# Performance work log

Measured on AMD Instinct MI355X. Metric: run time of the kernel, lower is better.

The kernel has to match this reference:

```python
import jax, jax.numpy as jnp
import numpy as np

DIM = 192          # token dim
INNER = 288        # round4(1.5*DIM)
NH_Q = 72          # headwise-proj heads (INNER // qkv_block_size)
DH_Q = 4           # per-head dim of q/k/v projections
NH_M = 4           # mLSTM heads (= qkv_block_size)
DH_M = 72          # INNER // NH_M
H, W = 32, 32
S = H * W
B = 8
KS = 3             # conv kernel size
EPS = 1e-6
LN_EPS = 1e-5


def setup_inputs() -> dict:
    key = jax.random.key(0)
    ks = jax.random.split(key, 12)
    sc = 0.02
    return {
        "x": jax.random.normal(ks[0], (B, S, DIM), jnp.float32),
        "proj_up_w": jax.random.normal(ks[1], (2 * INNER, DIM), jnp.float32) * sc,
        "q_w": jax.random.normal(ks[2], (NH_Q, DH_Q, DH_Q), jnp.float32) * sc,
        "k_w": jax.random.normal(ks[3], (NH_Q, DH_Q, DH_Q), jnp.float32) * sc,
        "v_w": jax.random.normal(ks[4], (NH_Q, DH_Q, DH_Q), jnp.float32) * sc,
        "conv_w": jax.random.normal(ks[5], (KS, KS, 1, INNER), jnp.float32) * sc,  # depthwise HWIO
        "ig_w": jax.random.normal(ks[6], (NH_M, 3 * INNER), jnp.float32) * sc,
        "ig_b": jax.random.normal(ks[7], (NH_M,), jnp.float32) * 0.1,
        "fg_w": jax.random.normal(ks[8], (NH_M, 3 * INNER), jnp.float32) * sc,
        "fg_b": jnp.linspace(3.0, 6.0, NH_M, dtype=jnp.float32),  # original fgate bias init
        "norm_w": jnp.ones((INNER,), jnp.float32),
        "skip": jnp.ones((INNER,), jnp.float32),
        "proj_down_w": jax.random.normal(ks[9], (DIM, INNER), jnp.float32) * sc,
    }


def _headwise(x, w):
    # x: (B,S,INNER), w: (NH_Q, DH_Q, DH_Q); block-diagonal linear per head
    xh = x.reshape(*x.shape[:-1], NH_Q, DH_Q)
    return jnp.einsum("bshd,hod->bsho", xh, w).reshape(x.shape)


def _mlstm_parallel(q, k, v, ig, fg):
    # q,k,v: (B,NH,S,DH); ig,fg: (B,NH,S) gate preactivations
    Ss, DH = q.shape[2], q.shape[3]
    logf = jax.nn.log_sigmoid(fg)                 # (B,NH,S)
    lfc = jnp.cumsum(logf, axis=-1)               # (B,NH,S)
    logF = lfc[..., :, None] - lfc[..., None, :]  # (B,NH,S,S): sum of logf over (j, i]
    mask = jnp.tril(jnp.ones((Ss, Ss), bool))
    logD = jnp.where(mask, logF + ig[..., None, :], -jnp.inf)
    maxD = jnp.max(logD, axis=-1, keepdims=True)  # (B,NH,S,1)
    Dm = jnp.exp(logD - maxD)
    qk = jnp.einsum("bnsd,bntd->bnst", q, k) / jnp.sqrt(jnp.float32(DH))
    Cm = qk * Dm
    normalizer = jnp.maximum(jnp.abs(Cm.sum(-1, keepdims=True)), jnp.exp(-maxD))
    return jnp.einsum("bnst,bntd->bnsd", Cm / (normalizer + EPS), v)


def reference(x, proj_up_w, q_w, k_w, v_w, conv_w, ig_w, ig_b, fg_w, fg_b,
              norm_w, skip, proj_down_w):
    Bb, Ss, _ = x.shape
    y = x @ proj_up_w.T                               # (B,S,2*INNER)
    x_m, z = y[..., :INNER], y[..., INNER:]
    # depthwise 2d conv over the (H,W) token grid
    xc = x_m.reshape(Bb, H, W, INNER)
    xc = jax.lax.conv_general_dilated(
        xc, conv_w, (1, 1), "SAME",
        dimension_numbers=("NHWC", "HWIO", "NHWC"), feature_group_count=INNER)
    xc = xc.reshape(Bb, Ss, INNER)
    xa = jax.nn.silu(xc)
    q = _headwise(xa, q_w)
    k = _headwise(xa, k_w)
    v = _headwise(x_m, v_w)
    gate_in = jnp.concatenate([q, k, v], axis=-1)      # (B,S,3*INNER)
    ig = (gate_in @ ig_w.T + ig_b).transpose(0, 2, 1)  # (B,NH_M,S)
    fg = (gate_in @ fg_w.T + fg_b).transpose(0, 2, 1)
    qh = q.reshape(Bb, Ss, NH_M, DH_M).transpose(0, 2, 1, 3)
    kh = k.reshape(Bb, Ss, NH_M, DH_M).transpose(0, 2, 1, 3)
    vh = v.reshape(Bb, Ss, NH_M, DH_M).transpose(0, 2, 1, 3)
    h = _mlstm_parallel(qh, kh, vh, ig, fg)            # (B,NH_M,S,DH_M)
    # per-head layernorm (group norm with NH_M groups), weight per channel
    mu = h.mean(-1, keepdims=True)
    var = h.var(-1, keepdims=True)
    hn = (h - mu) / jnp.sqrt(var + LN_EPS)
    hn = hn * norm_w.reshape(NH_M, 1, DH_M)[None]
    hn = hn.transpose(0, 2, 1, 3).reshape(Bb, Ss, INNER)
    h_skip = hn + skip * xa
    h_state = h_skip * jax.nn.silu(z)
    return h_state @ proj_down_w.T
```

## Files before the change

kernel.cpp:

```cpp
#include <hip/hip_runtime.h>
#include <math.h>

#define B_ 8
#define S_ 1024
#define INNER_ 288
#define NHM_ 4
#define DHM_ 72
#define H_ 32
#define W_ 32

typedef unsigned short ushort_t;
typedef unsigned int uint_t;
typedef __bf16 bf16x8 __attribute__((ext_vector_type(8)));
typedef float f32x4 __attribute__((ext_vector_type(4)));

__device__ __forceinline__ ushort_t f2bf(float f) {
  union { float f; unsigned u; } v; v.f = f;
  unsigned r = v.u + 0x7FFF + ((v.u >> 16) & 1);
  return (ushort_t)(r >> 16);
}
__device__ __forceinline__ float bf2f(ushort_t u) {
  union { unsigned u; float f; } v; v.u = ((unsigned)u) << 16;
  return v.f;
}
__device__ __forceinline__ void gl16(const void* g, void* l) {
  __builtin_amdgcn_global_load_lds(
      (const __attribute__((address_space(1))) void*)g,
      (__attribute__((address_space(3))) void*)l, 16, 0, 0);
}

__global__ __launch_bounds__(256) void prep_kernel(
    const float* __restrict__ x, const float* __restrict__ wupf,
    const float* __restrict__ wdnf,
    ushort_t* __restrict__ xbf, ushort_t* __restrict__ wup, ushort_t* __restrict__ wdn,
    ushort_t* __restrict__ hsb, ushort_t* __restrict__ qg, ushort_t* __restrict__ kg) {
  int s4 = blockIdx.x * 256 + threadIdx.x;
  const ushort4 z4 = {0, 0, 0, 0};
  if (s4 < 393216) {
    const int m = s4 / 48, k4 = (s4 % 48) * 4;
    const float4 v = *(const float4*)&x[(size_t)m * 192 + k4];
    ushort4 w = {f2bf(v.x), f2bf(v.y), f2bf(v.z), f2bf(v.w)};
    *(ushort4*)&xbf[(size_t)m * 192 + (k4 & ~63) + ((k4 & 63) ^ ((m & 7) << 3))] = w;
    return;
  }
  s4 -= 393216;
  if (s4 < 27648) {
    const int m = s4 / 48, k4 = (s4 % 48) * 4;
    const float4 v = *(const float4*)&wupf[(size_t)m * 192 + k4];
    ushort4 w = {f2bf(v.x), f2bf(v.y), f2bf(v.z), f2bf(v.w)};
    *(ushort4*)&wup[(size_t)m * 192 + (k4 & ~63) + ((k4 & 63) ^ ((m & 7) << 3))] = w;
    return;
  }
  s4 -= 27648;
  if (s4 < 15360) {
    const int m = s4 / 80, k4 = (s4 % 80) * 4;
    ushort4 w = z4;
    if (k4 < 288) {
      const float4 v = *(const float4*)&wdnf[(size_t)m * 288 + k4];
      w = (ushort4){f2bf(v.x), f2bf(v.y), f2bf(v.z), f2bf(v.w)};
    }
    *(ushort4*)&wdn[(size_t)m * 320 + (k4 & ~63) + ((k4 & 63) ^ ((m & 7) << 3))] = w;
    return;
  }
  s4 -= 15360;
  if (s4 < 131072) {
    const int p = s4 >> 4, j = s4 & 15;
    *(ushort4*)&hsb[(size_t)p * 320 + 256 + j * 4] = z4;
    return;
  }
  s4 -= 131072;
  if (s4 < 524288) {
    const int r = s4 >> 4, j = s4 & 15;
    *(ushort4*)&qg[(size_t)r * 128 + 64 + j * 4] = z4;
    return;
  }
  s4 -= 524288;
  {
    const int r = s4 >> 4, j = s4 & 15;
    *(ushort4*)&kg[(size_t)r * 128 + 64 + j * 4] = z4;
  }
}

template<int KT>
__global__ __launch_bounds__(256) void gemm_bf16(
    const ushort_t* __restrict__ A, const ushort_t* __restrict__ Bw,
    float* __restrict__ C, int N) {
  __shared__ __align__(16) ushort_t As[2][128 * 64];
  __shared__ __align__(16) ushort_t Bs[2][64 * 64];
  const int tid = threadIdx.x, lane = tid & 63, wv = tid >> 6;
  const int wm = wv >> 1, wn = wv & 1;
  const int cl = lane & 15, rowb = lane >> 4;
  const int m0 = blockIdx.y * 128, n0 = blockIdx.x * 64;
  const char* Ab = (const char*)A;
  const char* Bb = (const char*)Bw;

  auto stage = [&](int buf, int kt) {
    for (int u = wv; u < 24; u += 4) {
      if (u < 16) {
        const int o = u * 1024 + lane * 16;
        const int r = o >> 7, c = o & 127;
        gl16(Ab + ((size_t)(m0 + r) * KT + kt) * 128 + c, (char*)As[buf] + u * 1024);
      } else {
        const int o = (u - 16) * 1024 + lane * 16;
        const int r = o >> 7, c = o & 127;
        gl16(Bb + ((size_t)(n0 + r) * KT + kt) * 128 + c, (char*)Bs[buf] + (u - 16) * 1024);
      }
    }
  };

  f32x4 acc[4][2];
#pragma unroll
  for (int mi = 0; mi < 4; ++mi)
#pragma unroll
    for (int nj = 0; nj < 2; ++nj) acc[mi][nj] = (f32x4){0.f, 0.f, 0.f, 0.f};

  stage(0, 0);
  __syncthreads();
  for (int kt = 0; kt < KT; ++kt) {
    const int cur = kt & 1;
    if (kt + 1 < KT) stage(cur ^ 1, kt + 1);
#pragma unroll
    for (int ks = 0; ks < 2; ++ks) {
      bf16x8 af[4], bfr[2];
#pragma unroll
      for (int mi = 0; mi < 4; ++mi) {
        const int row = wm * 64 + mi * 16 + cl;
        af[mi] = *(const bf16x8*)((const char*)As[cur] + row * 128 +
                                  ((2 * (ks * 32 + rowb * 8)) ^ ((row & 7) << 4)));
      }
#pragma unroll
      for (int nj = 0; nj < 2; ++nj) {
        const int row = wn * 32 + nj * 16 + cl;
        bfr[nj] = *(const bf16x8*)((const char*)Bs[cur] + row * 128 +
                                   ((2 * (ks * 32 + rowb * 8)) ^ ((row & 7) << 4)));
      }
#pragma unroll
      for (int mi = 0; mi < 4; ++mi)
#pragma unroll
        for (int nj = 0; nj < 2; ++nj)
          acc[mi][nj] = __builtin_amdgcn_mfma_f32_16x16x32_bf16(af[mi], bfr[nj], acc[mi][nj], 0, 0, 0);
    }
    __syncthreads();
  }
#pragma unroll
  for (int mi = 0; mi < 4; ++mi)
#pragma unroll
    for (int i = 0; i < 4; ++i) {
      const size_t m = m0 + wm * 64 + mi * 16 + rowb * 4 + i;
#pragma unroll
      for (int nj = 0; nj < 2; ++nj)
        C[m * N + n0 + wn * 32 + nj * 16 + cl] = acc[mi][nj][i];
    }
}

__global__ __launch_bounds__(256) void conv_head_kernel(
    const float* __restrict__ y, const float* __restrict__ cw,
    const float* __restrict__ qw, const float* __restrict__ kw, const float* __restrict__ vw,
    float* __restrict__ xa,
    ushort_t* __restrict__ qg, ushort_t* __restrict__ kg, ushort_t* __restrict__ vg) {
  const int idx = blockIdx.x * 256 + threadIdx.x;
  const int hq = idx % 72;
  const int p = idx / 72;
  const int c = hq * 4;
  const int xx = p & 31, yy = (p >> 5) & 31, b = p >> 10, s = p & 1023;
  float4 acc = {0.f, 0.f, 0.f, 0.f};
  float4 xmv;
#pragma unroll
  for (int ky = 0; ky < 3; ++ky) {
    const int iy = yy + ky - 1;
    if (iy < 0 || iy >= H_) continue;
#pragma unroll
    for (int kx = 0; kx < 3; ++kx) {
      const int ix = xx + kx - 1;
      if (ix < 0 || ix >= W_) continue;
      const float4 v = *(const float4*)&y[((size_t)((b << 10) + (iy << 5) + ix)) * 576 + c];
      if (ky == 1 && kx == 1) xmv = v;
      const float4 w = *(const float4*)&cw[(ky * 3 + kx) * INNER_ + c];
      acc.x += v.x * w.x; acc.y += v.y * w.y; acc.z += v.z * w.z; acc.w += v.w * w.w;
    }
  }
  float4 xa4;
  xa4.x = acc.x / (1.f + __expf(-acc.x));
  xa4.y = acc.y / (1.f + __expf(-acc.y));
  xa4.z = acc.z / (1.f + __expf(-acc.z));
  xa4.w = acc.w / (1.f + __expf(-acc.w));
  *(float4*)&xa[(size_t)p * INNER_ + c] = xa4;
  float q[4], k2[4], v[4];
#pragma unroll
  for (int o = 0; o < 4; ++o) {
    const float4 wq = *(const float4*)&qw[hq * 16 + o * 4];
    const float4 wk = *(const float4*)&kw[hq * 16 + o * 4];
    const float4 wv4 = *(const float4*)&vw[hq * 16 + o * 4];
    q[o]  = wq.x * xa4.x + wq.y * xa4.y + wq.z * xa4.z + wq.w * xa4.w;
    k2[o] = wk.x * xa4.x + wk.y * xa4.y + wk.z * xa4.z + wk.w * xa4.w;
    v[o]  = wv4.x * xmv.x + wv4.y * xmv.y + wv4.z * xmv.z + wv4.w * xmv.w;
  }
  const int n = hq / 18, g = hq % 18;
  const int r = (b * 4 + n) * 1024 + s;
  const int swz = (s & 7) << 3;
  ushort4 uq = {f2bf(q[0]), f2bf(q[1]), f2bf(q[2]), f2bf(q[3])};
  ushort4 uk = {f2bf(k2[0]), f2bf(k2[1]), f2bf(k2[2]), f2bf(k2[3])};
  ushort4 uv = {f2bf(v[0]), f2bf(v[1]), f2bf(v[2]), f2bf(v[3])};
  *(ushort4*)&qg[(size_t)r * 128 + ((g * 4) ^ swz)] = uq;
  *(ushort4*)&kg[(size_t)r * 128 + ((g * 4) ^ swz)] = uk;
  *(ushort4*)&vg[(size_t)r * 72 + g * 4] = uv;
}

__global__ __launch_bounds__(256) void vtrans_kernel(
    const ushort_t* __restrict__ vg, ushort_t* __restrict__ vtg) {
  __shared__ ushort_t T[64][82];
  const int bn = blockIdx.x >> 4, tt = blockIdx.x & 15;
  const int s0 = tt << 6, tid = threadIdx.x;
  const uint_t* v32 = (const uint_t*)vg;
  for (int i = tid; i < 64 * 36; i += 256) {
    const int rr = i / 36, c2 = i % 36;
    *(uint_t*)&T[rr][c2 * 2] = v32[((size_t)(bn * 1024 + s0 + rr)) * 36 + c2];
  }
  __syncthreads();
  char* outb = (char*)(vtg + ((size_t)(bn * 16 + tt)) * 5120);
  for (int i = tid; i < 80 * 32; i += 256) {
    const int d = i >> 5, m = i & 31;
    uint_t val;
    if (d < 72) val = (uint_t)T[2 * m][d] | ((uint_t)T[2 * m + 1][d] << 16);
    else val = (d == 72) ? 0x3F803F80u : 0u;
    *(uint_t*)(outb + d * 128 + ((m * 4) ^ ((d & 7) << 4))) = val;
  }
}

__global__ __launch_bounds__(256) void gates_kernel(
    const ushort_t* __restrict__ qg, const ushort_t* __restrict__ kg, const ushort_t* __restrict__ vg,
    const float* __restrict__ igw, const float* __restrict__ igb,
    const float* __restrict__ fgw, const float* __restrict__ fgb,
    float* __restrict__ ig, float* __restrict__ fg) {
  const int gw = (blockIdx.x * 256 + threadIdx.x) >> 6;
  const int lane = threadIdx.x & 63;
  const int b = gw >> 10, s = gw & 1023;
  float iacc[4] = {}, facc[4] = {};
  for (int j = lane; j < 864; j += 64) {
    const int part = j / INNER_;
    const int c = j - part * INNER_;
    const int n = c / DHM_, d = c % DHM_;
    const size_t row = (size_t)(b * 4 + n) * 1024 + s;
    ushort_t u;
    if (part == 2)      u = vg[row * 72 + d];
    else {
      const size_t si = row * 128 + (d ^ ((row & 7) << 3));
      u = (part == 0) ? qg[si] : kg[si];
    }
    const float gv = bf2f(u);
#pragma unroll
    for (int nn = 0; nn < 4; ++nn) {
      iacc[nn] += gv * igw[nn * 864 + j];
      facc[nn] += gv * fgw[nn * 864 + j];
    }
  }
#pragma unroll
  for (int off = 32; off >= 1; off >>= 1) {
#pragma unroll
    for (int nn = 0; nn < 4; ++nn) {
      iacc[nn] += __shfl_xor(iacc[nn], off);
      facc[nn] += __shfl_xor(facc[nn], off);
    }
  }
  if (lane == 0) {
#pragma unroll
    for (int nn = 0; nn < 4; ++nn) {
      ig[((size_t)b * NHM_ + nn) * S_ + s] = iacc[nn] + igb[nn];
      fg[((size_t)b * NHM_ + nn) * S_ + s] = facc[nn] + fgb[nn];
    }
  }
}

__global__ __launch_bounds__(256) void scan_kernel(
    const float* __restrict__ fg, const float* __restrict__ ig,
    float* __restrict__ lfc, float* __restrict__ g, float* __restrict__ Mb) {
  __shared__ float sd[256];
  const int bn = blockIdx.x;
  const int tid = threadIdx.x;
  const float* fgp = &fg[(size_t)bn * S_];
  const float* igp = &ig[(size_t)bn * S_];
  float lf[4];
#pragma unroll
  for (int i = 0; i < 4; ++i) {
    const float f = fgp[tid * 4 + i];
    lf[i] = (f >= 0.f) ? -log1pf(expf(-f)) : (f - log1pf(expf(f)));
  }
  float p[4];
  p[0] = lf[0]; p[1] = p[0] + lf[1]; p[2] = p[1] + lf[2]; p[3] = p[2] + lf[3];
  sd[tid] = p[3];
  __syncthreads();
  for (int off = 1; off < 256; off <<= 1) {
    const float v = (tid >= off) ? sd[tid - off] : 0.f;
    __syncthreads();
    sd[tid] += v;
    __syncthreads();
  }
  const float excl = sd[tid] - p[3];
  float l[4];
#pragma unroll
  for (int i = 0; i < 4; ++i) {
    l[i] = excl + p[i];
    lfc[(size_t)bn * S_ + tid * 4 + i] = l[i];
  }
  float gv[4], pm[4];
#pragma unroll
  for (int i = 0; i < 4; ++i) gv[i] = igp[tid * 4 + i] - l[i];
  pm[0] = gv[0];
#pragma unroll
  for (int i = 1; i < 4; ++i) pm[i] = fmaxf(pm[i - 1], gv[i]);
  __syncthreads();
  sd[tid] = pm[3];
  __syncthreads();
  for (int off = 1; off < 256; off <<= 1) {
    const float v = (tid >= off) ? sd[tid - off] : -INFINITY;
    __syncthreads();
    sd[tid] = fmaxf(sd[tid], v);
    __syncthreads();
  }
  const float exclm = (tid > 0) ? sd[tid - 1] : -INFINITY;
#pragma unroll
  for (int i = 0; i < 4; ++i) {
    g[(size_t)bn * S_ + tid * 4 + i] = gv[i];
    Mb[(size_t)bn * S_ + tid * 4 + i] = fmaxf(exclm, pm[i]);
  }
}

__global__ __launch_bounds__(256) void mlstm_mfma(
    const ushort_t* __restrict__ qg, const ushort_t* __restrict__ kg,
    const ushort_t* __restrict__ vtg,
    const float* __restrict__ gb, const float* __restrict__ Mb, const float* __restrict__ lfc,
    const float* __restrict__ xa, const float* __restrict__ y,
    const float* __restrict__ normw, const float* __restrict__ skipw,
    ushort_t* __restrict__ hsb) {
  __shared__ __align__(16) ushort_t Ks[2][64 * 128];
  __shared__ __align__(16) ushort_t Vt[2][80 * 64];
  __shared__ __align__(16) ushort_t Ps[64 * 72];
  __shared__ float gs[1024];
  __shared__ float Ms_s[64], en_s[64];
  const int bi = blockIdx.x;
  const int bn = bi & 31;
  const int j = (bi >> 5) & 7;
  const int st = (bi >> 8) ? (15 - j) : j;
  const int s0 = st << 6;
  const int tid = threadIdx.x, lane = tid & 63, wv = tid >> 6;
  const int cl = lane & 15, rowb = lane >> 4;
  const char* kb = (const char*)(kg + (size_t)bn * 1024 * 128);
  const char* vtb = (const char*)(vtg + (size_t)bn * 16 * 5120);

  auto stage = [&](int buf, int tt) {
    const char* ks = kb + (size_t)tt * (64 * 256);
    const char* vs = vtb + (size_t)tt * 10240;
    for (int u = wv; u < 26; u += 4) {
      if (u < 16) gl16(ks + u * 1024 + lane * 16, (char*)Ks[buf] + u * 1024);
      else        gl16(vs + (u - 16) * 1024 + lane * 16, (char*)Vt[buf] + (u - 16) * 1024);
    }
  };

  stage(0, 0);
  *(float4*)&gs[tid * 4] = *(const float4*)&gb[(size_t)bn * S_ + tid * 4];
  if (tid < 64) {
    const float m = Mb[(size_t)bn * S_ + s0 + tid];
    Ms_s[tid] = m;
    en_s[tid] = __expf(-(lfc[(size_t)bn * S_ + s0 + tid] + m));
  }
  const int qrow = bn * 1024 + s0 + 16 * wv + cl;
  const ushort_t* qp = qg + (size_t)qrow * 128;
  const int qx = (qrow & 7) << 3;
  bf16x8 qf[3];
#pragma unroll
  for (int kk = 0; kk < 3; ++kk) qf[kk] = *(const bf16x8*)&qp[(kk * 32 + rowb * 8) ^ qx];

  f32x4 accv[5];
#pragma unroll
  for (int n0 = 0; n0 < 5; ++n0) accv[n0] = (f32x4){0.f, 0.f, 0.f, 0.f};
  const float rsc = 0.11785113019775793f;
  const int srl0 = 16 * wv + 4 * rowb;
  __syncthreads();

  for (int tt = 0; tt < st; ++tt) {
    const int cur = tt & 1;
    stage(cur ^ 1, tt + 1);
    const int t0 = tt << 6;
    f32x4 qk[4];
#pragma unroll
    for (int n0 = 0; n0 < 4; ++n0) qk[n0] = (f32x4){0.f, 0.f, 0.f, 0.f};
#pragma unroll
    for (int kk = 0; kk < 3; ++kk) {
#pragma unroll
      for (int n0 = 0; n0 < 4; ++n0) {
        const int rl = n0 * 16 + cl;
        const bf16x8 b = *(const bf16x8*)((const char*)Ks[cur] + rl * 256 +
                                          ((2 * (kk * 32 + rowb * 8)) ^ ((rl & 7) << 4)));
        qk[n0] = __builtin_amdgcn_mfma_f32_16x16x32_bf16(qf[kk], b, qk[n0], 0, 0, 0);
      }
    }
#pragma unroll
    for (int n0 = 0; n0 < 4; ++n0) {
      const float gtv = gs[t0 + n0 * 16 + cl];
#pragma unroll
      for (int i = 0; i < 4; ++i) {
        const float w = qk[n0][i] * rsc * __expf(gtv - Ms_s[srl0 + i]);
        Ps[(srl0 + i) * 72 + n0 * 16 + cl] = f2bf(w);
      }
    }
#pragma unroll
    for (int k0 = 0; k0 < 64; k0 += 32) {
      const bf16x8 a = *(const bf16x8*)&Ps[(16 * wv + cl) * 72 + k0 + rowb * 8];
#pragma unroll
      for (int n0 = 0; n0 < 5; ++n0) {
        const int d = n0 * 16 + cl;
        const bf16x8 b = *(const bf16x8*)((const char*)Vt[cur] + d * 128 +
                                          ((2 * (k0 + rowb * 8)) ^ ((d & 7) << 4)));
        accv[n0] = __builtin_amdgcn_mfma_f32_16x16x32_bf16(a, b, accv[n0], 0, 0, 0);
      }
    }
    __syncthreads();
  }
  {
    const int cur = st & 1;
    f32x4 qk[4];
#pragma unroll
    for (int n0 = 0; n0 < 4; ++n0) qk[n0] = (f32x4){0.f, 0.f, 0.f, 0.f};
#pragma unroll
    for (int kk = 0; kk < 3; ++kk) {
#pragma unroll
      for (int n0 = 0; n0 < 4; ++n0) {
        const int rl = n0 * 16 + cl;
        const bf16x8 b = *(const bf16x8*)((const char*)Ks[cur] + rl * 256 +
                                          ((2 * (kk * 32 + rowb * 8)) ^ ((rl & 7) << 4)));
        qk[n0] = __builtin_amdgcn_mfma_f32_16x16x32_bf16(qf[kk], b, qk[n0], 0, 0, 0);
      }
    }
#pragma unroll
    for (int n0 = 0; n0 < 4; ++n0) {
      const int tc = n0 * 16 + cl;
      const float gtv = gs[s0 + tc];
#pragma unroll
      for (int i = 0; i < 4; ++i) {
        const int srl = srl0 + i;
        const float w = (tc <= srl) ? qk[n0][i] * rsc * __expf(gtv - Ms_s[srl]) : 0.f;
        Ps[srl * 72 + n0 * 16 + cl] = f2bf(w);
      }
    }
#pragma unroll
    for (int k0 = 0; k0 < 64; k0 += 32) {
      const bf16x8 a = *(const bf16x8*)&Ps[(16 * wv + cl) * 72 + k0 + rowb * 8];
#pragma unroll
      for (int n0 = 0; n0 < 5; ++n0) {
        const int d = n0 * 16 + cl;
        const bf16x8 b = *(const bf16x8*)((const char*)Vt[cur] + d * 128 +
                                          ((2 * (k0 + rowb * 8)) ^ ((d & 7) << 4)));
        accv[n0] = __builtin_amdgcn_mfma_f32_16x16x32_bf16(a, b, accv[n0], 0, 0, 0);
      }
    }
  }
  float inv[4];
#pragma unroll
  for (int i = 0; i < 4; ++i) {
    const float rs = __shfl(accv[4][i], (lane & 48) + 8, 64);
    inv[i] = 1.f / (fmaxf(fabsf(rs), en_s[srl0 + i]) + 1e-6f);
  }
  const int b = bn >> 2, n = bn & 3;
  float nw[5], sw[5];
#pragma unroll
  for (int n0 = 0; n0 < 5; ++n0) {
    const int d = n0 * 16 + cl;
    nw[n0] = (d < 72) ? normw[n * 72 + d] : 0.f;
    sw[n0] = (d < 72) ? skipw[n * 72 + d] : 0.f;
  }
#pragma unroll
  for (int i = 0; i < 4; ++i) {
    const int srl = srl0 + i;
    const int p = (b << 10) + s0 + srl;
    float hv[5];
#pragma unroll
    for (int n0 = 0; n0 < 5; ++n0) hv[n0] = accv[n0][i] * inv[i];
    float hsum = hv[0] + hv[1] + hv[2] + hv[3] + ((cl < 8) ? hv[4] : 0.f);
#pragma unroll
    for (int m = 1; m < 16; m <<= 1) hsum += __shfl_xor(hsum, m);
    const float mean = hsum * (1.f / 72.f);
    float dsq = 0.f;
#pragma unroll
    for (int n0 = 0; n0 < 5; ++n0) {
      const int d = n0 * 16 + cl;
      const float dd = hv[n0] - mean;
      if (d < 72) dsq += dd * dd;
    }
#pragma unroll
    for (int m = 1; m < 16; m <<= 1) dsq += __shfl_xor(dsq, m);
    const float rstd = rsqrtf(dsq * (1.f / 72.f) + 1e-5f);
    const int pswz = (p & 7) << 3;
#pragma unroll
    for (int n0 = 0; n0 < 5; ++n0) {
      const int d = n0 * 16 + cl;
      if (d < 72) {
        const int c = n * 72 + d;
        const float hn = (hv[n0] - mean) * rstd * nw[n0];
        const float xav = xa[(size_t)p * INNER_ + c];
        const float z = y[(size_t)p * 576 + 288 + c];
        const float sz = z / (1.f + __expf(-z));
        hsb[(size_t)p * 320 + (c & ~63) + ((c & 63) ^ pswz)] = f2bf((hn + sw[n0] * xav) * sz);
      }
    }
  }
}

extern "C" void kernel_launch(void* const* d_in, const int* in_sizes, int n_in,
                              void* d_out, int out_size, void* d_ws, size_t ws_size,
                              hipStream_t stream) {
  const float* x           = (const float*)d_in[0];
  const float* proj_up_w   = (const float*)d_in[1];
  const float* q_w         = (const float*)d_in[2];
  const float* k_w         = (const float*)d_in[3];
  const float* v_w         = (const float*)d_in[4];
  const float* conv_w      = (const float*)d_in[5];
  const float* ig_w        = (const float*)d_in[6];
  const float* ig_b        = (const float*)d_in[7];
  const float* fg_w        = (const float*)d_in[8];
  const float* fg_b        = (const float*)d_in[9];
  const float* norm_w      = (const float*)d_in[10];
  const float* skipw       = (const float*)d_in[11];
  const float* proj_down_w = (const float*)d_in[12];
  float* out = (float*)d_out;

  float* ws = (float*)d_ws;
  float* y      = ws;
  float* xa     = y      + (size_t)8192 * 576;
  float* igb_   = xa     + (size_t)8192 * 288;
  float* fgb_   = igb_   + 32768;
  float* lfcb   = fgb_   + 32768;
  float* gbuf   = lfcb   + 32768;
  float* Mbuf   = gbuf   + 32768;
  ushort_t* qg  = (ushort_t*)(Mbuf + 32768);
  ushort_t* kg  = qg  + (size_t)32 * 1024 * 128;
  ushort_t* vg  = kg  + (size_t)32 * 1024 * 128;
  ushort_t* vtg = vg  + (size_t)32 * 1024 * 72;
  ushort_t* xbf = vtg + (size_t)32 * 16 * 5120;
  ushort_t* wup = xbf + (size_t)8192 * 192;
  ushort_t* wdn = wup + (size_t)576 * 192;
  ushort_t* hsb = wdn + (size_t)192 * 320;

  prep_kernel<<<6312, 256, 0, stream>>>(x, proj_up_w, proj_down_w,
                                        xbf, wup, wdn, hsb, qg, kg);
  gemm_bf16<3><<<dim3(9, 64), 256, 0, stream>>>(xbf, wup, y, 576);
  conv_head_kernel<<<(8192 * 72) / 256, 256, 0, stream>>>(
      y, conv_w, q_w, k_w, v_w, xa, qg, kg, vg);
  vtrans_kernel<<<512, 256, 0, stream>>>(vg, vtg);
  gates_kernel<<<8192 / 4, 256, 0, stream>>>(qg, kg, vg, ig_w, ig_b, fg_w, fg_b, igb_, fgb_);
  scan_kernel<<<B_ * NHM_, 256, 0, stream>>>(fgb_, igb_, lfcb, gbuf, Mbuf);
  mlstm_mfma<<<512, 256, 0, stream>>>(qg, kg, vtg, gbuf, Mbuf, lfcb,
                                      xa, y, norm_w, skipw, hsb);
  gemm_bf16<5><<<dim3(3, 64), 256, 0, stream>>>(hsb, wdn, out, 192);
}
```

Measured before the change: 168.9 us.

## Fuse mid-pipeline kernels into one cooperative kernel with grid syncs

Merges the conv/headwise, V transpose, gate projection, scan and mLSTM kernels into a single cooperative launch of 512 blocks, separated by grid-wide barriers and sharing one static shared-memory buffer. The aim is to remove four kernel launch boundaries and their idle gaps. In exchange, phases that used many more blocks (conv, gates) now run with grid-stride loops over 512 blocks, the scan phase occupies only 32 blocks while the rest wait at a barrier, and grid.sync adds its own cost.

```diff
diff --git a/kernel.cpp b/kernel.cpp
--- a/kernel.cpp
+++ b/kernel.cpp
@@ -1,5 +1,8 @@
 #include <hip/hip_runtime.h>
+#include <hip/hip_cooperative_groups.h>
 #include <math.h>
+
+namespace cg = cooperative_groups;
 
 #define B_ 8
 #define S_ 1024
@@ -153,353 +156,353 @@
     }
 }
 
-__global__ __launch_bounds__(256) void conv_head_kernel(
+__global__ __launch_bounds__(256, 2) void fused_mid(
     const float* __restrict__ y, const float* __restrict__ cw,
     const float* __restrict__ qw, const float* __restrict__ kw, const float* __restrict__ vw,
-    float* __restrict__ xa,
-    ushort_t* __restrict__ qg, ushort_t* __restrict__ kg, ushort_t* __restrict__ vg) {
-  const int idx = blockIdx.x * 256 + threadIdx.x;
-  const int hq = idx % 72;
-  const int p = idx / 72;
-  const int c = hq * 4;
-  const int xx = p & 31, yy = (p >> 5) & 31, b = p >> 10, s = p & 1023;
-  float4 acc = {0.f, 0.f, 0.f, 0.f};
-  float4 xmv;
-#pragma unroll
-  for (int ky = 0; ky < 3; ++ky) {
-    const int iy = yy + ky - 1;
-    if (iy < 0 || iy >= H_) continue;
-#pragma unroll
-    for (int kx = 0; kx < 3; ++kx) {
-      const int ix = xx + kx - 1;
-      if (ix < 0 || ix >= W_) continue;
-      const float4 v = *(const float4*)&y[((size_t)((b << 10) + (iy << 5) + ix)) * 576 + c];
-      if (ky == 1 && kx == 1) xmv = v;
-      const float4 w = *(const float4*)&cw[(ky * 3 + kx) * INNER_ + c];
-      acc.x += v.x * w.x; acc.y += v.y * w.y; acc.z += v.z * w.z; acc.w += v.w * w.w;
-    }
-  }
-  float4 xa4;
-  xa4.x = acc.x / (1.f + __expf(-acc.x));
-  xa4.y = acc.y / (1.f + __expf(-acc.y));
-  xa4.z = acc.z / (1.f + __expf(-acc.z));
-  xa4.w = acc.w / (1.f + __expf(-acc.w));
-  *(float4*)&xa[(size_t)p * INNER_ + c] = xa4;
-  float q[4], k2[4], v[4];
-#pragma unroll
-  for (int o = 0; o < 4; ++o) {
-    const float4 wq = *(const float4*)&qw[hq * 16 + o * 4];
-    const float4 wk = *(const float4*)&kw[hq * 16 + o * 4];
-    const float4 wv4 = *(const float4*)&vw[hq * 16 + o * 4];
-    q[o]  = wq.x * xa4.x + wq.y * xa4.y + wq.z * xa4.z + wq.w * xa4.w;
-    k2[o] = wk.x * xa4.x + wk.y * xa4.y + wk.z * xa4.z + wk.w * xa4.w;
-    v[o]  = wv4.x * xmv.x + wv4.y * xmv.y + wv4.z * xmv.z + wv4.w * xmv.w;
-  }
-  const int n = hq / 18, g = hq % 18;
-  const int r = (b * 4 + n) * 1024 + s;
-  const int swz = (s & 7) << 3;
-  ushort4 uq = {f2bf(q[0]), f2bf(q[1]), f2bf(q[2]), f2bf(q[3])};
-  ushort4 uk = {f2bf(k2[0]), f2bf(k2[1]), f2bf(k2[2]), f2bf(k2[3])};
-  ushort4 uv = {f2bf(v[0]), f2bf(v[1]), f2bf(v[2]), f2bf(v[3])};
-  *(ushort4*)&qg[(size_t)r * 128 + ((g * 4) ^ swz)] = uq;
-  *(ushort4*)&kg[(size_t)r * 128 + ((g * 4) ^ swz)] = uk;
-  *(ushort4*)&vg[(size_t)r * 72 + g * 4] = uv;
-}
-
-__global__ __launch_bounds__(256) void vtrans_kernel(
-    const ushort_t* __restrict__ vg, ushort_t* __restrict__ vtg) {
-  __shared__ ushort_t T[64][82];
-  const int bn = blockIdx.x >> 4, tt = blockIdx.x & 15;
-  const int s0 = tt << 6, tid = threadIdx.x;
-  const uint_t* v32 = (const uint_t*)vg;
-  for (int i = tid; i < 64 * 36; i += 256) {
-    const int rr = i / 36, c2 = i % 36;
-    *(uint_t*)&T[rr][c2 * 2] = v32[((size_t)(bn * 1024 + s0 + rr)) * 36 + c2];
-  }
-  __syncthreads();
-  char* outb = (char*)(vtg + ((size_t)(bn * 16 + tt)) * 5120);
-  for (int i = tid; i < 80 * 32; i += 256) {
-    const int d = i >> 5, m = i & 31;
-    uint_t val;
-    if (d < 72) val = (uint_t)T[2 * m][d] | ((uint_t)T[2 * m + 1][d] << 16);
-    else val = (d == 72) ? 0x3F803F80u : 0u;
-    *(uint_t*)(outb + d * 128 + ((m * 4) ^ ((d & 7) << 4))) = val;
-  }
-}
-
-__global__ __launch_bounds__(256) void gates_kernel(
-    const ushort_t* __restrict__ qg, const ushort_t* __restrict__ kg, const ushort_t* __restrict__ vg,
-    const float* __restrict__ igw, const float* __restrict__ igb,
-    const float* __restrict__ fgw, const float* __restrict__ fgb,
-    float* __restrict__ ig, float* __restrict__ fg) {
-  const int gw = (blockIdx.x * 256 + threadIdx.x) >> 6;
-  const int lane = threadIdx.x & 63;
-  const int b = gw >> 10, s = gw & 1023;
-  float iacc[4] = {}, facc[4] = {};
-  for (int j = lane; j < 864; j += 64) {
-    const int part = j / INNER_;
-    const int c = j - part * INNER_;
-    const int n = c / DHM_, d = c % DHM_;
-    const size_t row = (size_t)(b * 4 + n) * 1024 + s;
-    ushort_t u;
-    if (part == 2)      u = vg[row * 72 + d];
-    else {
-      const size_t si = row * 128 + (d ^ ((row & 7) << 3));
-      u = (part == 0) ? qg[si] : kg[si];
-    }
-    const float gv = bf2f(u);
-#pragma unroll
-    for (int nn = 0; nn < 4; ++nn) {
-      iacc[nn] += gv * igw[nn * 864 + j];
-      facc[nn] += gv * fgw[nn * 864 + j];
-    }
-  }
-#pragma unroll
-  for (int off = 32; off >= 1; off >>= 1) {
-#pragma unroll
-    for (int nn = 0; nn < 4; ++nn) {
-      iacc[nn] += __shfl_xor(iacc[nn], off);
-      facc[nn] += __shfl_xor(facc[nn], off);
-    }
-  }
-  if (lane == 0) {
-#pragma unroll
-    for (int nn = 0; nn < 4; ++nn) {
-      ig[((size_t)b * NHM_ + nn) * S_ + s] = iacc[nn] + igb[nn];
-      fg[((size_t)b * NHM_ + nn) * S_ + s] = facc[nn] + fgb[nn];
-    }
-  }
-}
-
-__global__ __launch_bounds__(256) void scan_kernel(
-    const float* __restrict__ fg, const float* __restrict__ ig,
-    float* __restrict__ lfc, float* __restrict__ g, float* __restrict__ Mb) {
-  __shared__ float sd[256];
-  const int bn = blockIdx.x;
-  const int tid = threadIdx.x;
-  const float* fgp = &fg[(size_t)bn * S_];
-  const float* igp = &ig[(size_t)bn * S_];
-  float lf[4];
-#pragma unroll
-  for (int i = 0; i < 4; ++i) {
-    const float f = fgp[tid * 4 + i];
-    lf[i] = (f >= 0.f) ? -log1pf(expf(-f)) : (f - log1pf(expf(f)));
-  }
-  float p[4];
-  p[0] = lf[0]; p[1] = p[0] + lf[1]; p[2] = p[1] + lf[2]; p[3] = p[2] + lf[3];
-  sd[tid] = p[3];
-  __syncthreads();
-  for (int off = 1; off < 256; off <<= 1) {
-    const float v = (tid >= off) ? sd[tid - off] : 0.f;
-    __syncthreads();
-    sd[tid] += v;
-    __syncthreads();
-  }
-  const float excl = sd[tid] - p[3];
-  float l[4];
-#pragma unroll
-  for (int i = 0; i < 4; ++i) {
-    l[i] = excl + p[i];
-    lfc[(size_t)bn * S_ + tid * 4 + i] = l[i];
-  }
-  float gv[4], pm[4];
-#pragma unroll
-  for (int i = 0; i < 4; ++i) gv[i] = igp[tid * 4 + i] - l[i];
-  pm[0] = gv[0];
-#pragma unroll
-  for (int i = 1; i < 4; ++i) pm[i] = fmaxf(pm[i - 1], gv[i]);
-  __syncthreads();
-  sd[tid] = pm[3];
-  __syncthreads();
-  for (int off = 1; off < 256; off <<= 1) {
-    const float v = (tid >= off) ? sd[tid - off] : -INFINITY;
-    __syncthreads();
-    sd[tid] = fmaxf(sd[tid], v);
-    __syncthreads();
-  }
-  const float exclm = (tid > 0) ? sd[tid - 1] : -INFINITY;
-#pragma unroll
-  for (int i = 0; i < 4; ++i) {
-    g[(size_t)bn * S_ + tid * 4 + i] = gv[i];
-    Mb[(size_t)bn * S_ + tid * 4 + i] = fmaxf(exclm, pm[i]);
-  }
-}
-
-__global__ __launch_bounds__(256) void mlstm_mfma(
-    const ushort_t* __restrict__ qg, const ushort_t* __restrict__ kg,
-    const ushort_t* __restrict__ vtg,
-    const float* __restrict__ gb, const float* __restrict__ Mb, const float* __restrict__ lfc,
-    const float* __restrict__ xa, const float* __restrict__ y,
+    const float* __restrict__ igw, const float* __restrict__ igbias,
+    const float* __restrict__ fgw, const float* __restrict__ fgbias,
+    float* __restrict__ xa, ushort_t* __restrict__ qg, ushort_t* __restrict__ kg,
+    ushort_t* __restrict__ vg, ushort_t* __restrict__ vtg,
+    float* __restrict__ igb_, float* __restrict__ fgb_, float* __restrict__ lfcb,
+    float* __restrict__ gbuf, float* __restrict__ Mbuf,
     const float* __restrict__ normw, const float* __restrict__ skipw,
     ushort_t* __restrict__ hsb) {
-  __shared__ __align__(16) ushort_t Ks[2][64 * 128];
-  __shared__ __align__(16) ushort_t Vt[2][80 * 64];
-  __shared__ __align__(16) ushort_t Ps[64 * 72];
-  __shared__ float gs[1024];
-  __shared__ float Ms_s[64], en_s[64];
-  const int bi = blockIdx.x;
-  const int bn = bi & 31;
-  const int j = (bi >> 5) & 7;
-  const int st = (bi >> 8) ? (15 - j) : j;
-  const int s0 = st << 6;
-  const int tid = threadIdx.x, lane = tid & 63, wv = tid >> 6;
-  const int cl = lane & 15, rowb = lane >> 4;
-  const char* kb = (const char*)(kg + (size_t)bn * 1024 * 128);
-  const char* vtb = (const char*)(vtg + (size_t)bn * 16 * 5120);
-
-  auto stage = [&](int buf, int tt) {
-    const char* ks = kb + (size_t)tt * (64 * 256);
-    const char* vs = vtb + (size_t)tt * 10240;
-    for (int u = wv; u < 26; u += 4) {
-      if (u < 16) gl16(ks + u * 1024 + lane * 16, (char*)Ks[buf] + u * 1024);
-      else        gl16(vs + (u - 16) * 1024 + lane * 16, (char*)Vt[buf] + (u - 16) * 1024);
-    }
-  };
-
-  stage(0, 0);
-  *(float4*)&gs[tid * 4] = *(const float4*)&gb[(size_t)bn * S_ + tid * 4];
-  if (tid < 64) {
-    const float m = Mb[(size_t)bn * S_ + s0 + tid];
-    Ms_s[tid] = m;
-    en_s[tid] = __expf(-(lfc[(size_t)bn * S_ + s0 + tid] + m));
-  }
-  const int qrow = bn * 1024 + s0 + 16 * wv + cl;
-  const ushort_t* qp = qg + (size_t)qrow * 128;
-  const int qx = (qrow & 7) << 3;
-  bf16x8 qf[3];
-#pragma unroll
-  for (int kk = 0; kk < 3; ++kk) qf[kk] = *(const bf16x8*)&qp[(kk * 32 + rowb * 8) ^ qx];
-
-  f32x4 accv[5];
-#pragma unroll
-  for (int n0 = 0; n0 < 5; ++n0) accv[n0] = (f32x4){0.f, 0.f, 0.f, 0.f};
-  const float rsc = 0.11785113019775793f;
-  const int srl0 = 16 * wv + 4 * rowb;
-  __syncthreads();
-
-  for (int tt = 0; tt < st; ++tt) {
-    const int cur = tt & 1;
-    stage(cur ^ 1, tt + 1);
-    const int t0 = tt << 6;
-    f32x4 qk[4];
-#pragma unroll
-    for (int n0 = 0; n0 < 4; ++n0) qk[n0] = (f32x4){0.f, 0.f, 0.f, 0.f};
-#pragma unroll
-    for (int kk = 0; kk < 3; ++kk) {
+  __shared__ __align__(16) unsigned char smem[67072];
+  cg::grid_group grid = cg::this_grid();
+  const int bi = blockIdx.x, tid = threadIdx.x;
+  const int lane = tid & 63, wv = tid >> 6;
+
+  for (int idx = bi * 256 + tid; idx < 8192 * 72; idx += 512 * 256) {
+    const int hq = idx % 72;
+    const int p = idx / 72;
+    const int c = hq * 4;
+    const int xx = p & 31, yy = (p >> 5) & 31, b = p >> 10, s = p & 1023;
+    float4 acc = {0.f, 0.f, 0.f, 0.f};
+    float4 xmv;
+#pragma unroll
+    for (int ky = 0; ky < 3; ++ky) {
+      const int iy = yy + ky - 1;
+      if (iy < 0 || iy >= H_) continue;
+#pragma unroll
+      for (int kx = 0; kx < 3; ++kx) {
+        const int ix = xx + kx - 1;
+        if (ix < 0 || ix >= W_) continue;
+        const float4 v = *(const float4*)&y[((size_t)((b << 10) + (iy << 5) + ix)) * 576 + c];
+        if (ky == 1 && kx == 1) xmv = v;
+        const float4 w = *(const float4*)&cw[(ky * 3 + kx) * INNER_ + c];
+        acc.x += v.x * w.x; acc.y += v.y * w.y; acc.z += v.z * w.z; acc.w += v.w * w.w;
+      }
+    }
+    float4 xa4;
+    xa4.x = acc.x / (1.f + __expf(-acc.x));
+    xa4.y = acc.y / (1.f + __expf(-acc.y));
+    xa4.z = acc.z / (1.f + __expf(-acc.z));
+    xa4.w = acc.w / (1.f + __expf(-acc.w));
+    *(float4*)&xa[(size_t)p * INNER_ + c] = xa4;
+    float q[4], k2[4], v[4];
+#pragma unroll
+    for (int o = 0; o < 4; ++o) {
+      const float4 wq = *(const float4*)&qw[hq * 16 + o * 4];
+      const float4 wk = *(const float4*)&kw[hq * 16 + o * 4];
+      const float4 wv4 = *(const float4*)&vw[hq * 16 + o * 4];
+      q[o]  = wq.x * xa4.x + wq.y * xa4.y + wq.z * xa4.z + wq.w * xa4.w;
+      k2[o] = wk.x * xa4.x + wk.y * xa4.y + wk.z * xa4.z + wk.w * xa4.w;
+      v[o]  = wv4.x * xmv.x + wv4.y * xmv.y + wv4.z * xmv.z + wv4.w * xmv.w;
+    }
+    const int n = hq / 18, g = hq % 18;
+    const int r = (b * 4 + n) * 1024 + s;
+    const int swz = (s & 7) << 3;
+    ushort4 uq = {f2bf(q[0]), f2bf(q[1]), f2bf(q[2]), f2bf(q[3])};
+    ushort4 uk = {f2bf(k2[0]), f2bf(k2[1]), f2bf(k2[2]), f2bf(k2[3])};
+    ushort4 uv = {f2bf(v[0]), f2bf(v[1]), f2bf(v[2]), f2bf(v[3])};
+    *(ushort4*)&qg[(size_t)r * 128 + ((g * 4) ^ swz)] = uq;
+    *(ushort4*)&kg[(size_t)r * 128 + ((g * 4) ^ swz)] = uk;
+    *(ushort4*)&vg[(size_t)r * 72 + g * 4] = uv;
+  }
+  grid.sync();
+
+  {
+    ushort_t (*T)[82] = (ushort_t (*)[82])smem;
+    const int bn = bi >> 4, tt = bi & 15;
+    const int s0 = tt << 6;
+    const uint_t* v32 = (const uint_t*)vg;
+    for (int i = tid; i < 64 * 36; i += 256) {
+      const int rr = i / 36, c2 = i % 36;
+      *(uint_t*)&T[rr][c2 * 2] = v32[((size_t)(bn * 1024 + s0 + rr)) * 36 + c2];
+    }
+    __syncthreads();
+    char* outb = (char*)(vtg + ((size_t)(bn * 16 + tt)) * 5120);
+    for (int i = tid; i < 80 * 32; i += 256) {
+      const int d = i >> 5, m = i & 31;
+      uint_t val;
+      if (d < 72) val = (uint_t)T[2 * m][d] | ((uint_t)T[2 * m + 1][d] << 16);
+      else val = (d == 72) ? 0x3F803F80u : 0u;
+      *(uint_t*)(outb + d * 128 + ((m * 4) ^ ((d & 7) << 4))) = val;
+    }
+  }
+  grid.sync();
+
+  for (int kk = 0; kk < 4; ++kk) {
+    const int gw = bi * 4 + wv + kk * 2048;
+    const int b = gw >> 10, s = gw & 1023;
+    float iacc[4] = {}, facc[4] = {};
+    for (int j = lane; j < 864; j += 64) {
+      const int part = j / INNER_;
+      const int c = j - part * INNER_;
+      const int n = c / DHM_, d = c % DHM_;
+      const size_t row = (size_t)(b * 4 + n) * 1024 + s;
+      ushort_t u;
+      if (part == 2)      u = vg[row * 72 + d];
+      else {
+        const size_t si = row * 128 + (d ^ ((row & 7) << 3));
+        u = (part == 0) ? qg[si] : kg[si];
+      }
+      const float gv = bf2f(u);
+#pragma unroll
+      for (int nn = 0; nn < 4; ++nn) {
+        iacc[nn] += gv * igw[nn * 864 + j];
+        facc[nn] += gv * fgw[nn * 864 + j];
+      }
+    }
+#pragma unroll
+    for (int off = 32; off >= 1; off >>= 1) {
+#pragma unroll
+      for (int nn = 0; nn < 4; ++nn) {
+        iacc[nn] += __shfl_xor(iacc[nn], off);
+        facc[nn] += __shfl_xor(facc[nn], off);
+      }
+    }
+    if (lane == 0) {
+#pragma unroll
+      for (int nn = 0; nn < 4; ++nn) {
+        igb_[((size_t)b * NHM_ + nn) * S_ + s] = iacc[nn] + igbias[nn];
+        fgb_[((size_t)b * NHM_ + nn) * S_ + s] = facc[nn] + fgbias[nn];
+      }
+    }
+  }
+  grid.sync();
+
+  if (bi < 32) {
+    float* sd = (float*)smem;
+    const int bn = bi;
+    const float* fgp = &fgb_[(size_t)bn * S_];
+    const float* igp = &igb_[(size_t)bn * S_];
+    float lf[4];
+#pragma unroll
+    for (int i = 0; i < 4; ++i) {
+      const float f = fgp[tid * 4 + i];
+      lf[i] = (f >= 0.f) ? -log1pf(expf(-f)) : (f - log1pf(expf(f)));
+    }
+    float p[4];
+    p[0] = lf[0]; p[1] = p[0] + lf[1]; p[2] = p[1] + lf[2]; p[3] = p[2] + lf[3];
+    sd[tid] = p[3];
+    __syncthreads();
+    for (int off = 1; off < 256; off <<= 1) {
+      const float v = (tid >= off) ? sd[tid - off] : 0.f;
+      __syncthreads();
+      sd[tid] += v;
+      __syncthreads();
+    }
+    const float excl = sd[tid] - p[3];
+    float l[4];
+#pragma unroll
+    for (int i = 0; i < 4; ++i) {
+      l[i] = excl + p[i];
+      lfcb[(size_t)bn * S_ + tid * 4 + i] = l[i];
+    }
+    float gv[4], pm[4];
+#pragma unroll
+    for (int i = 0; i < 4; ++i) gv[i] = igp[tid * 4 + i] - l[i];
+    pm[0] = gv[0];
+#pragma unroll
+    for (int i = 1; i < 4; ++i) pm[i] = fmaxf(pm[i - 1], gv[i]);
+    __syncthreads();
+    sd[tid] = pm[3];
+    __syncthreads();
+    for (int off = 1; off < 256; off <<= 1) {
+      const float v = (tid >= off) ? sd[tid - off] : -INFINITY;
+      __syncthreads();
+      sd[tid] = fmaxf(sd[tid], v);
+      __syncthreads();
+    }
+    const float exclm = (tid > 0) ? sd[tid - 1] : -INFINITY;
+#pragma unroll
+    for (int i = 0; i < 4; ++i) {
+      gbuf[(size_t)bn * S_ + tid * 4 + i] = gv[i];
+      Mbuf[(size_t)bn * S_ + tid * 4 + i] = fmaxf(exclm, pm[i]);
+    }
+  }
+  grid.sync();
+
+  {
+    ushort_t* Ks0 = (ushort_t*)smem;
+    ushort_t* Vt0 = (ushort_t*)(smem + 32768);
+    ushort_t* Ps  = (ushort_t*)(smem + 53248);
+    float* gs     = (float*)(smem + 62464);
+    float* Ms_s   = (float*)(smem + 66560);
+    float* en_s   = (float*)(smem + 66816);
+    const int bn = bi & 31;
+    const int j = (bi >> 5) & 7;
+    const int st = (bi >> 8) ? (15 - j) : j;
+    const int s0 = st << 6;
+    const int cl = lane & 15, rowb = lane >> 4;
+    const char* kb = (const char*)(kg + (size_t)bn * 1024 * 128);
+    const char* vtb = (const char*)(vtg + (size_t)bn * 16 * 5120);
+
+    auto stage = [&](int buf, int tt) {
+      const char* ks = kb + (size_t)tt * (64 * 256);
+      const char* vs = vtb + (size_t)tt * 10240;
+      for (int u = wv; u < 26; u += 4) {
+        if (u < 16) gl16(ks + u * 1024 + lane * 16, (char*)Ks0 + buf * 16384 + u * 1024);
+        else        gl16(vs + (u - 16) * 1024 + lane * 16, (char*)Vt0 + buf * 10240 + (u - 16) * 1024);
+      }
+    };
+
+    stage(0, 0);
+    *(float4*)&gs[tid * 4] = *(const float4*)&gbuf[(size_t)bn * S_ + tid * 4];
+    if (tid < 64) {
+      const float m = Mbuf[(size_t)bn * S_ + s0 + tid];
+      Ms_s[tid] = m;
+      en_s[tid] = __expf(-(lfcb[(size_t)bn * S_ + s0 + tid] + m));
+    }
+    const int qrow = bn * 1024 + s0 + 16 * wv + cl;
+    const ushort_t* qp = qg + (size_t)qrow * 128;
+    const int qx = (qrow & 7) << 3;
+    bf16x8 qf[3];
+#pragma unroll
+    for (int kk = 0; kk < 3; ++kk) qf[kk] = *(const bf16x8*)&qp[(kk * 32 + rowb * 8) ^ qx];
+
+    f32x4 accv[5];
+#pragma unroll
+    for (int n0 = 0; n0 < 5; ++n0) accv[n0] = (f32x4){0.f, 0.f, 0.f, 0.f};
+    const float rsc = 0.11785113019775793f;
+    const int srl0 = 16 * wv + 4 * rowb;
+    __syncthreads();
+
+    for (int tt = 0; tt < st; ++tt) {
+      const int cur = tt & 1;
+      stage(cur ^ 1, tt + 1);
+      const int t0 = tt << 6;
+      f32x4 qk[4];
+#pragma unroll
+      for (int n0 = 0; n0 < 4; ++n0) qk[n0] = (f32x4){0.f, 0.f, 0.f, 0.f};
+#pragma unroll
+      for (int kk = 0; kk < 3; ++kk) {
+#pragma unroll
+        for (int n0 = 0; n0 < 4; ++n0) {
+          const int rl = n0 * 16 + cl;
+          const bf16x8 b = *(const bf16x8*)((const char*)Ks0 + cur * 16384 + rl * 256 +
+                                            ((2 * (kk * 32 + rowb * 8)) ^ ((rl & 7) << 4)));
+          qk[n0] = __builtin_amdgcn_mfma_f32_16x16x32_bf16(qf[kk], b, qk[n0], 0, 0, 0);
+        }
+      }
 #pragma unroll
       for (int n0 = 0; n0 < 4; ++n0) {
-        const int rl = n0 * 16 + cl;
-        const bf16x8 b = *(const bf16x8*)((const char*)Ks[cur] + rl * 256 +
-                                          ((2 * (kk * 32 + rowb * 8)) ^ ((rl & 7) << 4)));
-        qk[n0] = __builtin_amdgcn_mfma_f32_16x16x32_bf16(qf[kk], b, qk[n0], 0, 0, 0);
-      }
-    }
-#pragma unroll
-    for (int n0 = 0; n0 < 4; ++n0) {
-      const float gtv = gs[t0 + n0 * 16 + cl];
-#pragma unroll
-      for (int i = 0; i < 4; ++i) {
-        const float w = qk[n0][i] * rsc * __expf(gtv - Ms_s[srl0 + i]);
-        Ps[(srl0 + i) * 72 + n0 * 16 + cl] = f2bf(w);
-      }
-    }
-#pragma unroll
-    for (int k0 = 0; k0 < 64; k0 += 32) {
-      const bf16x8 a = *(const bf16x8*)&Ps[(16 * wv + cl) * 72 + k0 + rowb * 8];
+        const float gtv = gs[t0 + n0 * 16 + cl];
+#pragma unroll
+        for (int i = 0; i < 4; ++i) {
+          const float w = qk[n0][i] * rsc * __expf(gtv - Ms_s[srl0 + i]);
+          Ps[(srl0 + i) * 72 + n0 * 16 + cl] = f2bf(w);
+        }
+      }
+#pragma unroll
+      for (int k0 = 0; k0 < 64; k0 += 32) {
+        const bf16x8 a = *(const bf16x8*)&Ps[(16 * wv + cl) * 72 + k0 + rowb * 8];
+#pragma unroll
+        for (int n0 = 0; n0 < 5; ++n0) {
+          const int d = n0 * 16 + cl;
+          const bf16x8 b = *(const bf16x8*)((const char*)Vt0 + cur * 10240 + d * 128 +
+                                            ((2 * (k0 + rowb * 8)) ^ ((d & 7) << 4)));
+          accv[n0] = __builtin_amdgcn_mfma_f32_16x16x32_bf16(a, b, accv[n0], 0, 0, 0);
+        }
+      }
+      __syncthreads();
+    }
+    {
+      const int cur = st & 1;
+      f32x4 qk[4];
+#pragma unroll
+      for (int n0 = 0; n0 < 4; ++n0) qk[n0] = (f32x4){0.f, 0.f, 0.f, 0.f};
+#pragma unroll
+      for (int kk = 0; kk < 3; ++kk) {
+#pragma unroll
+        for (int n0 = 0; n0 < 4; ++n0) {
+          const int rl = n0 * 16 + cl;
+          const bf16x8 b = *(const bf16x8*)((const char*)Ks0 + cur * 16384 + rl * 256 +
+                                            ((2 * (kk * 32 + rowb * 8)) ^ ((rl & 7) << 4)));
+          qk[n0] = __builtin_amdgcn_mfma_f32_16x16x32_bf16(qf[kk], b, qk[n0], 0, 0, 0);
+        }
+      }
+#pragma unroll
+      for (int n0 = 0; n0 < 4; ++n0) {
+        const int tc = n0 * 16 + cl;
+        const float gtv = gs[s0 + tc];
+#pragma unroll
+        for (int i = 0; i < 4; ++i) {
+          const int srl = srl0 + i;
+          const float w = (tc <= srl) ? qk[n0][i] * rsc * __expf(gtv - Ms_s[srl]) : 0.f;
+          Ps[srl * 72 + n0 * 16 + cl] = f2bf(w);
+        }
+      }
+#pragma unroll
+      for (int k0 = 0; k0 < 64; k0 += 32) {
+        const bf16x8 a = *(const bf16x8*)&Ps[(16 * wv + cl) * 72 + k0 + rowb * 8];
+#pragma unroll
+        for (int n0 = 0; n0 < 5; ++n0) {
+          const int d = n0 * 16 + cl;
+          const bf16x8 b = *(const bf16x8*)((const char*)Vt0 + cur * 10240 + d * 128 +
+                                            ((2 * (k0 + rowb * 8)) ^ ((d & 7) << 4)));
+          accv[n0] = __builtin_amdgcn_mfma_f32_16x16x32_bf16(a, b, accv[n0], 0, 0, 0);
+        }
+      }
+    }
+    float inv[4];
+#pragma unroll
+    for (int i = 0; i < 4; ++i) {
+      const float rs = __shfl(accv[4][i], (lane & 48) + 8, 64);
+      inv[i] = 1.f / (fmaxf(fabsf(rs), en_s[srl0 + i]) + 1e-6f);
+    }
+    const int b = bn >> 2, n = bn & 3;
+    float nw[5], sw[5];
+#pragma unroll
+    for (int n0 = 0; n0 < 5; ++n0) {
+      const int d = n0 * 16 + cl;
+      nw[n0] = (d < 72) ? normw[n * 72 + d] : 0.f;
+      sw[n0] = (d < 72) ? skipw[n * 72 + d] : 0.f;
+    }
+#pragma unroll
+    for (int i = 0; i < 4; ++i) {
+      const int srl = srl0 + i;
+      const int p = (b << 10) + s0 + srl;
+      float hv[5];
+#pragma unroll
+      for (int n0 = 0; n0 < 5; ++n0) hv[n0] = accv[n0][i] * inv[i];
+      float hsum = hv[0] + hv[1] + hv[2] + hv[3] + ((cl < 8) ? hv[4] : 0.f);
+#pragma unroll
+      for (int m = 1; m < 16; m <<= 1) hsum += __shfl_xor(hsum, m);
+      const float mean = hsum * (1.f / 72.f);
+      float dsq = 0.f;
 #pragma unroll
       for (int n0 = 0; n0 < 5; ++n0) {
         const int d = n0 * 16 + cl;
-        const bf16x8 b = *(const bf16x8*)((const char*)Vt[cur] + d * 128 +
-                                          ((2 * (k0 + rowb * 8)) ^ ((d & 7) << 4)));
-        accv[n0] = __builtin_amdgcn_mfma_f32_16x16x32_bf16(a, b, accv[n0], 0, 0, 0);
-      }
-    }
-    __syncthreads();
-  }
-  {
-    const int cur = st & 1;
-    f32x4 qk[4];
-#pragma unroll
-    for (int n0 = 0; n0 < 4; ++n0) qk[n0] = (f32x4){0.f, 0.f, 0.f, 0.f};
-#pragma unroll
-    for (int kk = 0; kk < 3; ++kk) {
-#pragma unroll
-      for (int n0 = 0; n0 < 4; ++n0) {
-        const int rl = n0 * 16 + cl;
-        const bf16x8 b = *(const bf16x8*)((const char*)Ks[cur] + rl * 256 +
-                                          ((2 * (kk * 32 + rowb * 8)) ^ ((rl & 7) << 4)));
-        qk[n0] = __builtin_amdgcn_mfma_f32_16x16x32_bf16(qf[kk], b, qk[n0], 0, 0, 0);
-      }
-    }
-#pragma unroll
-    for (int n0 = 0; n0 < 4; ++n0) {
-      const int tc = n0 * 16 + cl;
-      const float gtv = gs[s0 + tc];
-#pragma unroll
-      for (int i = 0; i < 4; ++i) {
-        const int srl = srl0 + i;
-        const float w = (tc <= srl) ? qk[n0][i] * rsc * __expf(gtv - Ms_s[srl]) : 0.f;
-        Ps[srl * 72 + n0 * 16 + cl] = f2bf(w);
-      }
-    }
-#pragma unroll
-    for (int k0 = 0; k0 < 64; k0 += 32) {
-      const bf16x8 a = *(const bf16x8*)&Ps[(16 * wv + cl) * 72 + k0 + rowb * 8];
+        const float dd = hv[n0] - mean;
+        if (d < 72) dsq += dd * dd;
+      }
+#pragma unroll
+      for (int m = 1; m < 16; m <<= 1) dsq += __shfl_xor(dsq, m);
+      const float rstd = rsqrtf(dsq * (1.f / 72.f) + 1e-5f);
+      const int pswz = (p & 7) << 3;
 #pragma unroll
       for (int n0 = 0; n0 < 5; ++n0) {
         const int d = n0 * 16 + cl;
-        const bf16x8 b = *(const bf16x8*)((const char*)Vt[cur] + d * 128 +
-                                          ((2 * (k0 + rowb * 8)) ^ ((d & 7) << 4)));
-        accv[n0] = __builtin_amdgcn_mfma_f32_16x16x32_bf16(a, b, accv[n0], 0, 0, 0);
-      }
-    }
-  }
-  float inv[4];
-#pragma unroll
-  for (int i = 0; i < 4; ++i) {
-    const float rs = __shfl(accv[4][i], (lane & 48) + 8, 64);
-    inv[i] = 1.f / (fmaxf(fabsf(rs), en_s[srl0 + i]) + 1e-6f);
-  }
-  const int b = bn >> 2, n = bn & 3;
-  float nw[5], sw[5];
-#pragma unroll
-  for (int n0 = 0; n0 < 5; ++n0) {
-    const int d = n0 * 16 + cl;
-    nw[n0] = (d < 72) ? normw[n * 72 + d] : 0.f;
-    sw[n0] = (d < 72) ? skipw[n * 72 + d] : 0.f;
-  }
-#pragma unroll
-  for (int i = 0; i < 4; ++i) {
-    const int srl = srl0 + i;
-    const int p = (b << 10) + s0 + srl;
-    float hv[5];
-#pragma unroll
-    for (int n0 = 0; n0 < 5; ++n0) hv[n0] = accv[n0][i] * inv[i];
-    float hsum = hv[0] + hv[1] + hv[2] + hv[3] + ((cl < 8) ? hv[4] : 0.f);
-#pragma unroll
-    for (int m = 1; m < 16; m <<= 1) hsum += __shfl_xor(hsum, m);
-    const float mean = hsum * (1.f / 72.f);
-    float dsq = 0.f;
-#pragma unroll
-    for (int n0 = 0; n0 < 5; ++n0) {
-      const int d = n0 * 16 + cl;
-      const float dd = hv[n0] - mean;
-      if (d < 72) dsq += dd * dd;
-    }
-#pragma unroll
-    for (int m = 1; m < 16; m <<= 1) dsq += __shfl_xor(dsq, m);
-    const float rstd = rsqrtf(dsq * (1.f / 72.f) + 1e-5f);
-    const int pswz = (p & 7) << 3;
-#pragma unroll
-    for (int n0 = 0; n0 < 5; ++n0) {
-      const int d = n0 * 16 + cl;
-      if (d < 72) {
-        const int c = n * 72 + d;
-        const float hn = (hv[n0] - mean) * rstd * nw[n0];
-        const float xav = xa[(size_t)p * INNER_ + c];
-        const float z = y[(size_t)p * 576 + 288 + c];
-        const float sz = z / (1.f + __expf(-z));
-        hsb[(size_t)p * 320 + (c & ~63) + ((c & 63) ^ pswz)] = f2bf((hn + sw[n0] * xav) * sz);
+        if (d < 72) {
+          const int c = n * 72 + d;
+          const float hn = (hv[n0] - mean) * rstd * nw[n0];
+          const float xav = xa[(size_t)p * INNER_ + c];
+          const float z = y[(size_t)p * 576 + 288 + c];
+          const float sz = z / (1.f + __expf(-z));
+          hsb[(size_t)p * 320 + (c & ~63) + ((c & 63) ^ pswz)] = f2bf((hn + sw[n0] * xav) * sz);
+        }
       }
     }
   }
@@ -543,12 +546,15 @@
   prep_kernel<<<6312, 256, 0, stream>>>(x, proj_up_w, proj_down_w,
                                         xbf, wup, wdn, hsb, qg, kg);
   gemm_bf16<3><<<dim3(9, 64), 256, 0, stream>>>(xbf, wup, y, 576);
-  conv_head_kernel<<<(8192 * 72) / 256, 256, 0, stream>>>(
-      y, conv_w, q_w, k_w, v_w, xa, qg, kg, vg);
-  vtrans_kernel<<<512, 256, 0, stream>>>(vg, vtg);
-  gates_kernel<<<8192 / 4, 256, 0, stream>>>(qg, kg, vg, ig_w, ig_b, fg_w, fg_b, igb_, fgb_);
-  scan_kernel<<<B_ * NHM_, 256, 0, stream>>>(fgb_, igb_, lfcb, gbuf, Mbuf);
-  mlstm_mfma<<<512, 256, 0, stream>>>(qg, kg, vtg, gbuf, Mbuf, lfcb,
-                                      xa, y, norm_w, skipw, hsb);
+  {
+    const float* y_ = y;
+    void* args[] = {
+      (void*)&y_, (void*)&conv_w, (void*)&q_w, (void*)&k_w, (void*)&v_w,
+      (void*)&ig_w, (void*)&ig_b, (void*)&fg_w, (void*)&fg_b,
+      (void*)&xa, (void*)&qg, (void*)&kg, (void*)&vg, (void*)&vtg,
+      (void*)&igb_, (void*)&fgb_, (void*)&lfcb, (void*)&gbuf, (void*)&Mbuf,
+      (void*)&norm_w, (void*)&skipw, (void*)&hsb};
+    hipLaunchCooperativeKernel((void*)fused_mid, dim3(512), dim3(256), args, 0, stream);
+  }
   gemm_bf16<5><<<dim3(3, 64), 256, 0, stream>>>(hsb, wdn, out, 192);
 }
```

Result: slower. 437.3 us (+158.9%).
